# Performance work log

Measured on AMD Instinct MI355X. Metric: run time of the kernel, lower is better.

## Reference

```python
import jax, jax.numpy as jnp
import numpy as np
import math

N_HEADS = 16
N_BLOCK = 4
EPS = 1e-5


def _layernorm(h, g, b):
    mu = jnp.mean(h, axis=-1, keepdims=True)
    var = jnp.var(h, axis=-1, keepdims=True)
    return (h - mu) / jnp.sqrt(var + EPS) * g + b


def _sinusoidal_pe(S, D, dtype):
    pos = jnp.arange(S, dtype=jnp.float32)[:, None]                      # [S,1]
    div = jnp.exp(jnp.arange(0, D, 2, dtype=jnp.float32) * (-math.log(10000.0) / D))
    pe = jnp.zeros((S, D), dtype=jnp.float32)
    pe = pe.at[:, 0::2].set(jnp.sin(pos * div))
    pe = pe.at[:, 1::2].set(jnp.cos(pos * div))
    return pe.astype(dtype)


def setup_inputs() -> dict:
    key = jax.random.key(0)
    ks = jax.random.split(key, 10)
    V, D, Hf, B, S = 32000, 1024, 4096, 4, 1024
    s = 0.02
    return {
        'x': jax.random.randint(ks[0], (B, S), 0, V, dtype=jnp.int32),
        'emb_W': jax.random.normal(ks[1], (V, D), jnp.float32) * s,
        'q_W': jax.random.normal(ks[2], (D, D), jnp.float32) * s,
        'k_W': jax.random.normal(ks[3], (D, D), jnp.float32) * s,
        'v_W': jax.random.normal(ks[4], (D, D), jnp.float32) * s,
        'o_W': jax.random.normal(ks[5], (D, D), jnp.float32) * s,
        'ln0_g': jnp.ones((D,), jnp.float32),
        'ln0_b': jnp.zeros((D,), jnp.float32),
        'ln1_g': jnp.ones((D,), jnp.float32),
        'ln1_b': jnp.zeros((D,), jnp.float32),
        'ffn_W1': jax.random.normal(ks[6], (Hf, D), jnp.float32) * s,
        'ffn_b1': jnp.zeros((Hf,), jnp.float32),
        'ffn_W2': jax.random.normal(ks[7], (D, Hf), jnp.float32) * s,
        'ffn_b2': jnp.zeros((D,), jnp.float32),
        'out_W': jax.random.normal(ks[8], (V, D), jnp.float32) * s,
        'out_b': jnp.zeros((32000,), jnp.float32),
    }


def reference(x, emb_W, q_W, k_W, v_W, o_W, ln0_g, ln0_b, ln1_g, ln1_b,
              ffn_W1, ffn_b1, ffn_W2, ffn_b2, out_W, out_b):
    B, S = x.shape
    D = emb_W.shape[1]
    hd = D // N_HEADS
    # token embedding * sqrt(d_model) + sinusoidal PE (dropout is eval-mode identity)
    h = emb_W[x] * jnp.asarray(math.sqrt(D), emb_W.dtype)
    h = h + _sinusoidal_pe(S, D, h.dtype)[None]
    causal = jnp.tril(jnp.ones((S, S), dtype=bool))                      # [S,S]
    scale = 1.0 / math.sqrt(hd)

    for _ in range(N_BLOCK):  # weights shared across blocks, as in the source
        # attention sublayer; Resudial_Connections is x + LN(x)
        a_in = h + _layernorm(h, ln0_g, ln0_b)
        q = (a_in @ q_W.T).reshape(B, S, N_HEADS, hd).transpose(0, 2, 1, 3)
        k = (a_in @ k_W.T).reshape(B, S, N_HEADS, hd).transpose(0, 2, 1, 3)
        v = (a_in @ v_W.T).reshape(B, S, N_HEADS, hd).transpose(0, 2, 1, 3)
        scores = jnp.einsum('bhqd,bhkd->bhqk', q, k) * scale
        scores = jnp.where(causal, scores, -jnp.inf)
        attn = jax.nn.softmax(scores, axis=-1)
        o = jnp.einsum('bhqk,bhkd->bhqd', attn, v)
        o = o.transpose(0, 2, 1, 3).reshape(B, S, D) @ o_W.T
        h = h + o
        # FFN sublayer (intended Linear-ReLU-Linear)
        f_in = h + _layernorm(h, ln1_g, ln1_b)
        ff = jax.nn.relu(f_in @ ffn_W1.T + ffn_b1) @ ffn_W2.T + ffn_b2
        h = h + ff

    return h @ out_W.T + out_b                                           # [B,S,V]
```

## Files before the change

kernel.cpp:

```cpp
#include <hip/hip_runtime.h>
#include <hip/hip_bf16.h>
#include <math.h>

typedef __bf16 bf16_t;
typedef __bf16 bf16x8 __attribute__((ext_vector_type(8)));
typedef __bf16 bf16x4 __attribute__((ext_vector_type(4)));
typedef float  f32x4  __attribute__((ext_vector_type(4)));

#define MFMA_BF16(a, b, c) __builtin_amdgcn_mfma_f32_16x16x32_bf16((a), (b), (c), 0, 0, 0)

typedef const void __attribute__((address_space(1)))* gas_ptr;
typedef void       __attribute__((address_space(3)))* las_ptr;

__device__ __forceinline__ void gload_lds16(const void* g, void* l) {
  __builtin_amdgcn_global_load_lds((gas_ptr)g, (las_ptr)l, 16, 0, 0);
}

static constexpr int B_ = 4, S_ = 1024, D_ = 1024, HF_ = 4096, V_ = 32000;
static constexpr int NH_ = 16, HD_ = 64;
static constexpr int TOK_ = B_ * S_;

__global__ __launch_bounds__(256) void cvt_f32_bf16(const float* __restrict__ in,
                                                    bf16_t* __restrict__ out, int n4) {
  int i = blockIdx.x * 256 + threadIdx.x;
  if (i < n4) {
    float4 v = ((const float4*)in)[i];
    bf16x4 o;
    o[0] = (bf16_t)v.x; o[1] = (bf16_t)v.y; o[2] = (bf16_t)v.z; o[3] = (bf16_t)v.w;
    ((bf16x4*)out)[i] = o;
  }
}

__global__ __launch_bounds__(256) void pe_kernel(float* __restrict__ pe) {
  const int s = blockIdx.x;
  for (int i = threadIdx.x; i < D_ / 2; i += 256) {
    float div = expf((2.0f * (float)i) * (-9.210340371976184f / (float)D_));
    float a = (float)s * div;
    pe[(size_t)s * D_ + 2 * i]     = sinf(a);
    pe[(size_t)s * D_ + 2 * i + 1] = cosf(a);
  }
}

__global__ __launch_bounds__(256) void embed_kernel(const int* __restrict__ x,
                                                    const float* __restrict__ embW,
                                                    const float* __restrict__ pe,
                                                    float* __restrict__ h) {
  int i = blockIdx.x * 256 + threadIdx.x;
  int token = i >> 8;
  int c4 = i & 255;
  int idx = x[token];
  float4 e = ((const float4*)(embW + (size_t)idx * D_))[c4];
  float4 p = ((const float4*)(pe + (size_t)(token & (S_ - 1)) * D_))[c4];
  float4 o;
  o.x = e.x * 32.0f + p.x; o.y = e.y * 32.0f + p.y;
  o.z = e.z * 32.0f + p.z; o.w = e.w * 32.0f + p.w;
  ((float4*)(h + (size_t)token * D_))[c4] = o;
}

__global__ __launch_bounds__(256) void ln_res_kernel(const float* __restrict__ h,
                                                     const float* __restrict__ gamma,
                                                     const float* __restrict__ beta,
                                                     bf16_t* __restrict__ out) {
  const int row = blockIdx.x;
  const int tid = threadIdx.x;
  const float4 v = ((const float4*)(h + (size_t)row * D_))[tid];
  float s  = v.x + v.y + v.z + v.w;
  float s2 = v.x * v.x + v.y * v.y + v.z * v.z + v.w * v.w;
#pragma unroll
  for (int m = 1; m < 64; m <<= 1) {
    s  += __shfl_xor(s, m, 64);
    s2 += __shfl_xor(s2, m, 64);
  }
  __shared__ float red[2][4];
  const int wave = tid >> 6, lane = tid & 63;
  if (lane == 0) { red[0][wave] = s; red[1][wave] = s2; }
  __syncthreads();
  s  = red[0][0] + red[0][1] + red[0][2] + red[0][3];
  s2 = red[1][0] + red[1][1] + red[1][2] + red[1][3];
  const float mu   = s * (1.0f / D_);
  const float rstd = rsqrtf(s2 * (1.0f / D_) - mu * mu + 1e-5f);
  const float4 g4 = ((const float4*)gamma)[tid];
  const float4 b4 = ((const float4*)beta)[tid];
  bf16x4 o;
  o[0] = (bf16_t)(v.x + (v.x - mu) * rstd * g4.x + b4.x);
  o[1] = (bf16_t)(v.y + (v.y - mu) * rstd * g4.y + b4.y);
  o[2] = (bf16_t)(v.z + (v.z - mu) * rstd * g4.z + b4.z);
  o[3] = (bf16_t)(v.w + (v.w - mu) * rstd * g4.w + b4.w);
  ((bf16x4*)(out + (size_t)row * D_))[tid] = o;
}

template <int EPI>
__global__ __launch_bounds__(512, 4) void gemm_sq(
    const bf16_t* __restrict__ A, const bf16_t* __restrict__ W, int N, int K,
    float* __restrict__ fout, const float* __restrict__ bias, bf16_t* __restrict__ bout,
    bf16_t* __restrict__ qb, bf16_t* __restrict__ kb, bf16_t* __restrict__ vtb) {
  __shared__ char lds[2][32768];

  const int tid = threadIdx.x;
  const int wave = tid >> 6, lane = tid & 63;
  const int row16 = lane & 15, kgrp = lane >> 4;
  const int wm = wave >> 2, wn = wave & 3;

  const int nb = gridDim.x;
  const int logical = (blockIdx.x & 7) * (nb >> 3) + (blockIdx.x >> 3);
  const int m0 = (logical & 31) << 7;
  const int n0 = (logical >> 5) << 7;
  const size_t K2 = (size_t)K * 2;

  const int lr = lane >> 3;
  const int swz = ((lane & 7) * 16) ^ (lr << 4);
  const char* gA = (const char*)A + (size_t)(m0 + wave * 8 + lr) * K2 + swz;
  const char* gB = (const char*)W + (size_t)(n0 + wave * 8 + lr) * K2 + swz;
  char* const ldsc = &lds[0][0];
  const int dW = wave * 1024;

#define STG_A(v)                                                  \
  { char* d_ = ldsc + (((v) & 1) << 15) + dW;                     \
    const char* g_ = gA + (size_t)(v) * 128;                      \
    gload_lds16(g_, d_); gload_lds16(g_ + 64 * K2, d_ + 8192); }
#define STG_B(v)                                                  \
  { char* d_ = ldsc + (((v) & 1) << 15) + 16384 + dW;             \
    const char* g_ = gB + (size_t)(v) * 128;                      \
    gload_lds16(g_, d_); gload_lds16(g_ + 64 * K2, d_ + 8192); }

  const int colx0 = (kgrp * 16) ^ ((row16 & 7) << 4);
  const int colx1 = (64 + kgrp * 16) ^ ((row16 & 7) << 4);
  int aoff[4], boff[2];
#pragma unroll
  for (int mf = 0; mf < 4; mf++) aoff[mf] = (wm * 64 + mf * 16 + row16) * 128;
#pragma unroll
  for (int nf = 0; nf < 2; nf++) boff[nf] = 16384 + (nf * 64 + wn * 16 + row16) * 128;

#define GATE()                                        \
  __builtin_amdgcn_s_barrier();                       \
  asm volatile("s_waitcnt lgkmcnt(0)" ::: "memory");  \
  __builtin_amdgcn_sched_barrier(0);

  f32x4 acc[4][2] = {};
  bf16x8 af[4][2], bfr[2];
  const int NT = K >> 6;

  STG_A(0); STG_B(0); STG_A(1);
  asm volatile("s_waitcnt vmcnt(2)" ::: "memory");
  __builtin_amdgcn_s_barrier();

  for (int t = 0; t < NT; ++t) {
    const char* bufp = ldsc + ((t & 1) << 15);
#pragma unroll
    for (int mf = 0; mf < 4; mf++) {
      af[mf][0] = *(const bf16x8*)(bufp + aoff[mf] + colx0);
      af[mf][1] = *(const bf16x8*)(bufp + aoff[mf] + colx1);
    }
    bfr[0] = *(const bf16x8*)(bufp + boff[0] + colx0);
    bfr[1] = *(const bf16x8*)(bufp + boff[0] + colx1);
    if (t + 1 < NT) STG_B(t + 1);
    GATE();
    __builtin_amdgcn_s_setprio(1);
#pragma unroll
    for (int mf = 0; mf < 4; mf++) {
      acc[mf][0] = MFMA_BF16(af[mf][0], bfr[0], acc[mf][0]);
      acc[mf][0] = MFMA_BF16(af[mf][1], bfr[1], acc[mf][0]);
    }
    __builtin_amdgcn_s_setprio(0);
    __builtin_amdgcn_s_barrier();
    bfr[0] = *(const bf16x8*)(bufp + boff[1] + colx0);
    bfr[1] = *(const bf16x8*)(bufp + boff[1] + colx1);
    if (t + 2 < NT) STG_A(t + 2);
    GATE();
    __builtin_amdgcn_s_setprio(1);
#pragma unroll
    for (int mf = 0; mf < 4; mf++) {
      acc[mf][1] = MFMA_BF16(af[mf][0], bfr[0], acc[mf][1]);
      acc[mf][1] = MFMA_BF16(af[mf][1], bfr[1], acc[mf][1]);
    }
    __builtin_amdgcn_s_setprio(0);
    if (t + 2 < NT)      { asm volatile("s_waitcnt vmcnt(2)" ::: "memory"); }
    else if (t + 1 < NT) { asm volatile("s_waitcnt vmcnt(0)" ::: "memory"); }
    __builtin_amdgcn_s_barrier();
  }
#undef STG_A
#undef STG_B
#undef GATE

#pragma unroll
  for (int mf = 0; mf < 4; mf++) {
    const int rowb = m0 + wm * 64 + mf * 16 + kgrp * 4;
#pragma unroll
    for (int nf = 0; nf < 2; nf++) {
      const int col = n0 + nf * 64 + wn * 16 + row16;
#pragma unroll
      for (int r = 0; r < 4; r++) {
        const float v = acc[mf][nf][r];
        const int rr2 = rowb + r;
        if constexpr (EPI == 0) {
          const int bb = rr2 >> 10, s = rr2 & 1023;
          if (col < 1024) {
            const int hh = col >> 6, d = col & 63;
            qb[(((size_t)(bb * NH_ + hh)) * S_ + s) * HD_ + d] = (bf16_t)(v * 0.125f);
          } else if (col < 2048) {
            const int c = col - 1024, hh = c >> 6, d = c & 63;
            kb[(((size_t)(bb * NH_ + hh)) * S_ + s) * HD_ + d] = (bf16_t)v;
          } else {
            const int c = col - 2048, hh = c >> 6, d = c & 63;
            vtb[(((size_t)(bb * NH_ + hh)) * HD_ + d) * S_ + s] = (bf16_t)v;
          }
        } else if constexpr (EPI == 1) {
          fout[(size_t)rr2 * N + col] += v;
        } else if constexpr (EPI == 2) {
          bout[(size_t)rr2 * N + col] = (bf16_t)fmaxf(v + bias[col], 0.0f);
        } else {
          fout[(size_t)rr2 * N + col] += v + bias[col];
        }
      }
    }
  }
}

template <int EPI>
__global__ __launch_bounds__(512, 1) void gemm_pipe(
    const bf16_t* __restrict__ A, const bf16_t* __restrict__ W, int N, int K,
    float* __restrict__ fout, const float* __restrict__ bias) {
  __shared__ char lds[2][65536];

  const int tid = threadIdx.x;
  const int wave = tid >> 6, lane = tid & 63;
  const int row16 = lane & 15, kgrp = lane >> 4;
  const int wm = wave >> 2, wn = wave & 3;

  const int nb = gridDim.x;
  const int logical = (blockIdx.x & 7) * (nb >> 3) + (blockIdx.x >> 3);
  const int m0 = (logical & 15) << 8;
  const int n0 = (logical >> 4) << 8;
  const size_t K2 = (size_t)K * 2;

  const int lr = lane >> 3;
  const int swz = ((lane & 7) * 16) ^ (lr << 4);
  const int rA = wave * 8 + lr;
  const char* gAr = (const char*)A + (size_t)(m0 + rA) * K2 + swz;
  const int rB = (wave < 4 ? wave * 8 : 64 + (wave - 4) * 8) + lr;
  const char* gBr = (const char*)W + (size_t)(n0 + rB) * K2 + swz;
  char* const ldsc = &lds[0][0];
  const int dAw = wave * 1024;
  const int dBw = 32768 + (wave < 4 ? wave * 1024 : 8192 + (wave - 4) * 1024);

#define STG_AM03(v)                                                     \
  { char* d_ = ldsc + (((v) & 1) << 16) + dAw;                          \
    const char* g_ = gAr + (size_t)(v) * 128;                           \
    gload_lds16(g_, d_); gload_lds16(g_ + 128 * K2, d_ + 16384); }
#define STG_AM47(v)                                                     \
  { char* d_ = ldsc + (((v) & 1) << 16) + dAw + 8192;                   \
    const char* g_ = gAr + (size_t)(v) * 128 + 64 * K2;                 \
    gload_lds16(g_, d_); gload_lds16(g_ + 128 * K2, d_ + 16384); }
#define STG_BN01(v)                                                     \
  { char* d_ = ldsc + (((v) & 1) << 16) + dBw;                          \
    const char* g_ = gBr + (size_t)(v) * 128;                           \
    gload_lds16(g_, d_); gload_lds16(g_ + 128 * K2, d_ + 16384); }
#define STG_BN23(v)                                                     \
  { char* d_ = ldsc + (((v) & 1) << 16) + dBw + 4096;                   \
    const char* g_ = gBr + (size_t)(v) * 128 + 32 * K2;                 \
    gload_lds16(g_, d_); gload_lds16(g_ + 128 * K2, d_ + 16384); }

  const int colx0 = (kgrp * 16) ^ ((row16 & 7) << 4);
  const int colx1 = (64 + kgrp * 16) ^ ((row16 & 7) << 4);
  const int aA0 = (wm * 128 + row16) * 128 + colx0;
  const int aA1 = (wm * 128 + row16) * 128 + colx1;
  const int bA0 = 32768 + (wn * 64 + row16) * 128 + colx0;
  const int bA1 = 32768 + (wn * 64 + row16) * 128 + colx1;

#define LD_A(mh)                                                          \
  _Pragma("unroll") for (int m_ = 0; m_ < 4; m_++) {                      \
    af[m_][0] = *(const bf16x8*)(bufp + aA0 + (mh) * 8192 + m_ * 2048);   \
    af[m_][1] = *(const bf16x8*)(bufp + aA1 + (mh) * 8192 + m_ * 2048);   \
  }
#define LD_B(BF, nh)                                                      \
  _Pragma("unroll") for (int n_ = 0; n_ < 2; n_++) {                      \
    BF[n_][0] = *(const bf16x8*)(bufp + bA0 + (nh) * 4096 + n_ * 2048);   \
    BF[n_][1] = *(const bf16x8*)(bufp + bA1 + (nh) * 4096 + n_ * 2048);   \
  }
#define GATE()                                        \
  __builtin_amdgcn_s_barrier();                       \
  asm volatile("s_waitcnt lgkmcnt(0)" ::: "memory");  \
  __builtin_amdgcn_sched_barrier(0);
#define PH_MFMA(MB, NB, BF)                                                    \
  __builtin_amdgcn_s_setprio(1);                                               \
  _Pragma("unroll") for (int kh_ = 0; kh_ < 2; kh_++)                          \
    _Pragma("unroll") for (int m_ = 0; m_ < 4; m_++)                           \
      _Pragma("unroll") for (int n_ = 0; n_ < 2; n_++)                         \
          acc[(MB) + m_][(NB) + n_] =                                          \
              MFMA_BF16(af[m_][kh_], BF[n_][kh_], acc[(MB) + m_][(NB) + n_]);  \
  __builtin_amdgcn_s_setprio(0);

  f32x4 acc[8][4] = {};
  bf16x8 af[4][2], bfA[2][2], bfB[2][2];
  const int NT = K >> 6;

  STG_AM03(0); STG_BN01(0); STG_AM47(0); STG_BN23(0);
  if (NT > 1) { STG_AM03(1); STG_BN01(1); }
  if (NT > 1) { asm volatile("s_waitcnt vmcnt(8)" ::: "memory"); }
  else        { asm volatile("s_waitcnt vmcnt(4)" ::: "memory"); }
  __builtin_amdgcn_s_barrier();

  for (int t = 0; t < NT; ++t) {
    const char* bufp = ldsc + ((t & 1) << 16);
    LD_A(0);
    LD_B(bfA, 0);
    if (t + 1 < NT) STG_AM47(t + 1);
    GATE();
    PH_MFMA(0, 0, bfA);
    if (t + 1 < NT) { asm volatile("s_waitcnt vmcnt(6)" ::: "memory"); }
    else            { asm volatile("s_waitcnt vmcnt(0)" ::: "memory"); }
    __builtin_amdgcn_s_barrier();
    LD_B(bfB, 1);
    if (t + 1 < NT) STG_BN23(t + 1);
    GATE();
    PH_MFMA(0, 2, bfB);
    __builtin_amdgcn_s_barrier();
    LD_A(1);
    if (t + 2 < NT) STG_AM03(t + 2);
    GATE();
    PH_MFMA(4, 2, bfB);
    __builtin_amdgcn_s_barrier();
    if (t + 2 < NT) STG_BN01(t + 2);
    __builtin_amdgcn_s_barrier();
    __builtin_amdgcn_sched_barrier(0);
    PH_MFMA(4, 0, bfA);
    if (t + 2 < NT)      { asm volatile("s_waitcnt vmcnt(8)" ::: "memory"); }
    else if (t + 1 < NT) { asm volatile("s_waitcnt vmcnt(4)" ::: "memory"); }
    __builtin_amdgcn_s_barrier();
  }
#undef STG_AM03
#undef STG_AM47
#undef STG_BN01
#undef STG_BN23
#undef LD_A
#undef LD_B
#undef GATE
#undef PH_MFMA

#pragma unroll
  for (int m = 0; m < 8; m++) {
    const int rowb = m0 + wm * 128 + m * 16 + kgrp * 4;
#pragma unroll
    for (int n = 0; n < 4; n++) {
      const int col = n0 + wn * 64 + n * 16 + row16;
#pragma unroll
      for (int r = 0; r < 4; r++) {
        fout[(size_t)(rowb + r) * N + col] = acc[m][n][r] + bias[col];
      }
    }
  }
}

__global__ __launch_bounds__(256, 3) void attn_flash(const bf16_t* __restrict__ qg,
                                                     const bf16_t* __restrict__ kg,
                                                     const bf16_t* __restrict__ vtg,
                                                     bf16_t* __restrict__ aout) {
  const int nb = gridDim.x;
  const int logical = ((blockIdx.x & 7) * (nb >> 3)) + (blockIdx.x >> 3);
  const int qtile = logical & 15;
  const int bh    = logical >> 4;
  const int tid = threadIdx.x;
  const int wave = tid >> 6, lane = tid & 63;
  const int row16 = lane & 15, kgrp = lane >> 4;
  const int q0 = qtile * 64 + wave * 16;

  const bf16_t* qb = qg + (size_t)bh * S_ * HD_;
  const bf16_t* kb = kg + (size_t)bh * S_ * HD_;
  const bf16_t* vb = vtg + (size_t)bh * HD_ * S_;

  const bf16x8 qf0 = *(const bf16x8*)&qb[(size_t)(q0 + row16) * HD_ + kgrp * 8];
  const bf16x8 qf1 = *(const bf16x8*)&qb[(size_t)(q0 + row16) * HD_ + 32 + kgrp * 8];

  f32x4 accO[4] = {};
  float mrun[4] = {-1e30f, -1e30f, -1e30f, -1e30f};
  float lrun[4] = {0.f, 0.f, 0.f, 0.f};

  __shared__ char sP[4][2048];
  char* const sw = &sP[wave][0];

  const int NTt = qtile + 1;

  bf16x8 kf[4][2];
#pragma unroll
  for (int q = 0; q < 4; q++) {
    kf[q][0] = *(const bf16x8*)&kb[(size_t)(q * 16 + row16) * HD_ + kgrp * 8];
    kf[q][1] = *(const bf16x8*)&kb[(size_t)(q * 16 + row16) * HD_ + 32 + kgrp * 8];
  }

  for (int t = 0; t < NTt; ++t) {
    const int k0 = t * 64;
    f32x4 sc[4];
#pragma unroll
    for (int q = 0; q < 4; q++) {
      f32x4 z = {};
      z = MFMA_BF16(qf0, kf[q][0], z);
      sc[q] = MFMA_BF16(qf1, kf[q][1], z);
    }
    bf16x8 vf[4][2];
#pragma unroll
    for (int d = 0; d < 4; d++) {
      vf[d][0] = *(const bf16x8*)&vb[(size_t)(d * 16 + row16) * S_ + k0 + kgrp * 8];
      vf[d][1] = *(const bf16x8*)&vb[(size_t)(d * 16 + row16) * S_ + k0 + 32 + kgrp * 8];
    }
    const bool diag = (k0 + 64 > q0);
    float p[4][4];
#pragma unroll
    for (int r = 0; r < 4; r++) {
      const int qglob = q0 + kgrp * 4 + r;
      float s0 = sc[0][r], s1 = sc[1][r], s2 = sc[2][r], s3 = sc[3][r];
      if (diag) {
        s0 = (k0 + row16 <= qglob) ? s0 : -1e30f;
        s1 = (k0 + 16 + row16 <= qglob) ? s1 : -1e30f;
        s2 = (k0 + 32 + row16 <= qglob) ? s2 : -1e30f;
        s3 = (k0 + 48 + row16 <= qglob) ? s3 : -1e30f;
      }
      float tmax = fmaxf(fmaxf(s0, s1), fmaxf(s2, s3));
#pragma unroll
      for (int msk = 1; msk < 16; msk <<= 1) tmax = fmaxf(tmax, __shfl_xor(tmax, msk, 64));
      const float mnew  = fmaxf(mrun[r], tmax);
      const float alpha = __expf(mrun[r] - mnew);
      const float e0 = __expf(s0 - mnew);
      const float e1 = __expf(s1 - mnew);
      const float e2 = __expf(s2 - mnew);
      const float e3 = __expf(s3 - mnew);
      float ls = (e0 + e1) + (e2 + e3);
#pragma unroll
      for (int msk = 1; msk < 16; msk <<= 1) ls += __shfl_xor(ls, msk, 64);
      lrun[r] = lrun[r] * alpha + ls;
      mrun[r] = mnew;
#pragma unroll
      for (int d = 0; d < 4; d++) accO[d][r] *= alpha;
      p[r][0] = e0; p[r][1] = e1; p[r][2] = e2; p[r][3] = e3;
    }
    if (t + 1 < NTt) {
      const int k0n = k0 + 64;
#pragma unroll
      for (int q = 0; q < 4; q++) {
        kf[q][0] = *(const bf16x8*)&kb[(size_t)(k0n + q * 16 + row16) * HD_ + kgrp * 8];
        kf[q][1] = *(const bf16x8*)&kb[(size_t)(k0n + q * 16 + row16) * HD_ + 32 + kgrp * 8];
      }
    }
#pragma unroll
    for (int r = 0; r < 4; r++) {
      const int prow = kgrp * 4 + r;
      const int px = (prow & 7) << 4;
#pragma unroll
      for (int q = 0; q < 4; q++) {
        *(bf16_t*)(sw + prow * 128 + (((q * 16 + row16) * 2) ^ px)) = (bf16_t)p[r][q];
      }
    }
    const int rx = (row16 & 7) << 4;
    const bf16x8 pf0 = *(const bf16x8*)(sw + row16 * 128 + ((kgrp * 16) ^ rx));
    const bf16x8 pf1 = *(const bf16x8*)(sw + row16 * 128 + ((64 + kgrp * 16) ^ rx));
#pragma unroll
    for (int d = 0; d < 4; d++) {
      accO[d] = MFMA_BF16(pf0, vf[d][0], accO[d]);
      accO[d] = MFMA_BF16(pf1, vf[d][1], accO[d]);
    }
  }

  const int b = bh >> 4, hh = bh & 15;
#pragma unroll
  for (int d = 0; d < 4; d++)
#pragma unroll
    for (int r = 0; r < 4; r++) {
      const int tok = b * S_ + q0 + kgrp * 4 + r;
      aout[(size_t)tok * D_ + hh * HD_ + d * 16 + row16] = (bf16_t)(accO[d][r] / lrun[r]);
    }
}

extern "C" void kernel_launch(void* const* d_in, const int* in_sizes, int n_in,
                              void* d_out, int out_size, void* d_ws, size_t ws_size,
                              hipStream_t stream) {
  const int*   x      = (const int*)d_in[0];
  const float* emb_W  = (const float*)d_in[1];
  const float* q_W    = (const float*)d_in[2];
  const float* k_W    = (const float*)d_in[3];
  const float* v_W    = (const float*)d_in[4];
  const float* o_W    = (const float*)d_in[5];
  const float* ln0_g  = (const float*)d_in[6];
  const float* ln0_b  = (const float*)d_in[7];
  const float* ln1_g  = (const float*)d_in[8];
  const float* ln1_b  = (const float*)d_in[9];
  const float* ffn_W1 = (const float*)d_in[10];
  const float* ffn_b1 = (const float*)d_in[11];
  const float* ffn_W2 = (const float*)d_in[12];
  const float* ffn_b2 = (const float*)d_in[13];
  const float* out_W  = (const float*)d_in[14];
  const float* out_b  = (const float*)d_in[15];
  float* out = (float*)d_out;

  char* p = (char*)d_ws;
  auto take = [&](size_t n) { char* r = p; p += (n + 255) & ~(size_t)255; return r; };
  float*  pe    = (float*)take((size_t)S_ * D_ * 4);
  float*  h     = (float*)take((size_t)TOK_ * D_ * 4);
  bf16_t* ain   = (bf16_t*)take((size_t)TOK_ * D_ * 2);
  bf16_t* attno = (bf16_t*)take((size_t)TOK_ * D_ * 2);
  bf16_t* qb    = (bf16_t*)take((size_t)B_ * NH_ * S_ * HD_ * 2);
  bf16_t* kb    = (bf16_t*)take((size_t)B_ * NH_ * S_ * HD_ * 2);
  bf16_t* vtb   = (bf16_t*)take((size_t)B_ * NH_ * S_ * HD_ * 2);
  bf16_t* ff    = (bf16_t*)take((size_t)TOK_ * HF_ * 2);
  bf16_t* qkvW  = (bf16_t*)take((size_t)3 * D_ * D_ * 2);
  bf16_t* oWb   = (bf16_t*)take((size_t)D_ * D_ * 2);
  bf16_t* W1b   = (bf16_t*)take((size_t)HF_ * D_ * 2);
  bf16_t* W2b   = (bf16_t*)take((size_t)D_ * HF_ * 2);
  bf16_t* outWb = (bf16_t*)take((size_t)V_ * D_ * 2);

  cvt_f32_bf16<<<1024, 256, 0, stream>>>(q_W, qkvW, D_ * D_ / 4);
  cvt_f32_bf16<<<1024, 256, 0, stream>>>(k_W, qkvW + (size_t)D_ * D_, D_ * D_ / 4);
  cvt_f32_bf16<<<1024, 256, 0, stream>>>(v_W, qkvW + (size_t)2 * D_ * D_, D_ * D_ / 4);
  cvt_f32_bf16<<<1024, 256, 0, stream>>>(o_W, oWb, D_ * D_ / 4);
  cvt_f32_bf16<<<4096, 256, 0, stream>>>(ffn_W1, W1b, HF_ * D_ / 4);
  cvt_f32_bf16<<<4096, 256, 0, stream>>>(ffn_W2, W2b, D_ * HF_ / 4);
  cvt_f32_bf16<<<32000, 256, 0, stream>>>(out_W, outWb, V_ * D_ / 4);

  pe_kernel<<<S_, 256, 0, stream>>>(pe);
  embed_kernel<<<TOK_ * D_ / 4 / 256, 256, 0, stream>>>(x, emb_W, pe, h);

  for (int blk = 0; blk < 4; blk++) {
    ln_res_kernel<<<TOK_, 256, 0, stream>>>(h, ln0_g, ln0_b, ain);
    gemm_sq<0><<<32 * (3 * D_ / 128), 512, 0, stream>>>(
        ain, qkvW, 3 * D_, D_, nullptr, nullptr, nullptr, qb, kb, vtb);
    attn_flash<<<16 * B_ * NH_, 256, 0, stream>>>(qb, kb, vtb, attno);
    gemm_sq<1><<<32 * (D_ / 128), 512, 0, stream>>>(
        attno, oWb, D_, D_, h, nullptr, nullptr, nullptr, nullptr, nullptr);
    ln_res_kernel<<<TOK_, 256, 0, stream>>>(h, ln1_g, ln1_b, ain);
    gemm_sq<2><<<32 * (HF_ / 128), 512, 0, stream>>>(
        ain, W1b, HF_, D_, nullptr, ffn_b1, ff, nullptr, nullptr, nullptr);
    gemm_sq<3><<<32 * (D_ / 128), 512, 0, stream>>>(
        ff, W2b, D_, HF_, h, ffn_b2, nullptr, nullptr, nullptr, nullptr);
  }

  cvt_f32_bf16<<<4096, 256, 0, stream>>>(h, ain, TOK_ * D_ / 4);
  gemm_pipe<4><<<16 * (V_ / 256), 512, 0, stream>>>(
      ain, outWb, V_, D_, out, out_b);
}
```

Measured before the change: 1.537 ms.

## Replace pipelined vocab GEMM with gemm_sq and compute softmax row sums via MFMA

Removes the specialized 256x256 gemm_pipe kernel and runs the final vocab projection through the generic gemm_sq template, adding an EPI=4 store-with-bias epilogue. In flash attention, the per-row sum of exponentials is now accumulated by MFMA against a vector of ones instead of cross-lane shuffle reductions. The final normalization uses a reciprocal multiply. The row sums now come from the bf16-rounded probabilities, which matches the values used for P·V. The larger vocab GEMM may lose the tuned pipelining and the bigger tile reuse it had before.

Result: slower. 1.652 ms (+7.5%).

```diff
diff --git a/kernel.cpp b/kernel.cpp
--- a/kernel.cpp
+++ b/kernel.cpp
@@ -208,144 +208,11 @@
           fout[(size_t)rr2 * N + col] += v;
         } else if constexpr (EPI == 2) {
           bout[(size_t)rr2 * N + col] = (bf16_t)fmaxf(v + bias[col], 0.0f);
+        } else if constexpr (EPI == 3) {
+          fout[(size_t)rr2 * N + col] += v + bias[col];
         } else {
-          fout[(size_t)rr2 * N + col] += v + bias[col];
+          fout[(size_t)rr2 * N + col] = v + bias[col];
         }
-      }
-    }
-  }
-}
-
-template <int EPI>
-__global__ __launch_bounds__(512, 1) void gemm_pipe(
-    const bf16_t* __restrict__ A, const bf16_t* __restrict__ W, int N, int K,
-    float* __restrict__ fout, const float* __restrict__ bias) {
-  __shared__ char lds[2][65536];
-
-  const int tid = threadIdx.x;
-  const int wave = tid >> 6, lane = tid & 63;
-  const int row16 = lane & 15, kgrp = lane >> 4;
-  const int wm = wave >> 2, wn = wave & 3;
-
-  const int nb = gridDim.x;
-  const int logical = (blockIdx.x & 7) * (nb >> 3) + (blockIdx.x >> 3);
-  const int m0 = (logical & 15) << 8;
-  const int n0 = (logical >> 4) << 8;
-  const size_t K2 = (size_t)K * 2;
-
-  const int lr = lane >> 3;
-  const int swz = ((lane & 7) * 16) ^ (lr << 4);
-  const int rA = wave * 8 + lr;
-  const char* gAr = (const char*)A + (size_t)(m0 + rA) * K2 + swz;
-  const int rB = (wave < 4 ? wave * 8 : 64 + (wave - 4) * 8) + lr;
-  const char* gBr = (const char*)W + (size_t)(n0 + rB) * K2 + swz;
-  char* const ldsc = &lds[0][0];
-  const int dAw = wave * 1024;
-  const int dBw = 32768 + (wave < 4 ? wave * 1024 : 8192 + (wave - 4) * 1024);
-
-#define STG_AM03(v)                                                     \
-  { char* d_ = ldsc + (((v) & 1) << 16) + dAw;                          \
-    const char* g_ = gAr + (size_t)(v) * 128;                           \
-    gload_lds16(g_, d_); gload_lds16(g_ + 128 * K2, d_ + 16384); }
-#define STG_AM47(v)                                                     \
-  { char* d_ = ldsc + (((v) & 1) << 16) + dAw + 8192;                   \
-    const char* g_ = gAr + (size_t)(v) * 128 + 64 * K2;                 \
-    gload_lds16(g_, d_); gload_lds16(g_ + 128 * K2, d_ + 16384); }
-#define STG_BN01(v)                                                     \
-  { char* d_ = ldsc + (((v) & 1) << 16) + dBw;                          \
-    const char* g_ = gBr + (size_t)(v) * 128;                           \
-    gload_lds16(g_, d_); gload_lds16(g_ + 128 * K2, d_ + 16384); }
-#define STG_BN23(v)                                                     \
-  { char* d_ = ldsc + (((v) & 1) << 16) + dBw + 4096;                   \
-    const char* g_ = gBr + (size_t)(v) * 128 + 32 * K2;                 \
-    gload_lds16(g_, d_); gload_lds16(g_ + 128 * K2, d_ + 16384); }
-
-  const int colx0 = (kgrp * 16) ^ ((row16 & 7) << 4);
-  const int colx1 = (64 + kgrp * 16) ^ ((row16 & 7) << 4);
-  const int aA0 = (wm * 128 + row16) * 128 + colx0;
-  const int aA1 = (wm * 128 + row16) * 128 + colx1;
-  const int bA0 = 32768 + (wn * 64 + row16) * 128 + colx0;
-  const int bA1 = 32768 + (wn * 64 + row16) * 128 + colx1;
-
-#define LD_A(mh)                                                          \
-  _Pragma("unroll") for (int m_ = 0; m_ < 4; m_++) {                      \
-    af[m_][0] = *(const bf16x8*)(bufp + aA0 + (mh) * 8192 + m_ * 2048);   \
-    af[m_][1] = *(const bf16x8*)(bufp + aA1 + (mh) * 8192 + m_ * 2048);   \
-  }
-#define LD_B(BF, nh)                                                      \
-  _Pragma("unroll") for (int n_ = 0; n_ < 2; n_++) {                      \
-    BF[n_][0] = *(const bf16x8*)(bufp + bA0 + (nh) * 4096 + n_ * 2048);   \
-    BF[n_][1] = *(const bf16x8*)(bufp + bA1 + (nh) * 4096 + n_ * 2048);   \
-  }
-#define GATE()                                        \
-  __builtin_amdgcn_s_barrier();                       \
-  asm volatile("s_waitcnt lgkmcnt(0)" ::: "memory");  \
-  __builtin_amdgcn_sched_barrier(0);
-#define PH_MFMA(MB, NB, BF)                                                    \
-  __builtin_amdgcn_s_setprio(1);                                               \
-  _Pragma("unroll") for (int kh_ = 0; kh_ < 2; kh_++)                          \
-    _Pragma("unroll") for (int m_ = 0; m_ < 4; m_++)                           \
-      _Pragma("unroll") for (int n_ = 0; n_ < 2; n_++)                         \
-          acc[(MB) + m_][(NB) + n_] =                                          \
-              MFMA_BF16(af[m_][kh_], BF[n_][kh_], acc[(MB) + m_][(NB) + n_]);  \
-  __builtin_amdgcn_s_setprio(0);
-
-  f32x4 acc[8][4] = {};
-  bf16x8 af[4][2], bfA[2][2], bfB[2][2];
-  const int NT = K >> 6;
-
-  STG_AM03(0); STG_BN01(0); STG_AM47(0); STG_BN23(0);
-  if (NT > 1) { STG_AM03(1); STG_BN01(1); }
-  if (NT > 1) { asm volatile("s_waitcnt vmcnt(8)" ::: "memory"); }
-  else        { asm volatile("s_waitcnt vmcnt(4)" ::: "memory"); }
-  __builtin_amdgcn_s_barrier();
-
-  for (int t = 0; t < NT; ++t) {
-    const char* bufp = ldsc + ((t & 1) << 16);
-    LD_A(0);
-    LD_B(bfA, 0);
-    if (t + 1 < NT) STG_AM47(t + 1);
-    GATE();
-    PH_MFMA(0, 0, bfA);
-    if (t + 1 < NT) { asm volatile("s_waitcnt vmcnt(6)" ::: "memory"); }
-    else            { asm volatile("s_waitcnt vmcnt(0)" ::: "memory"); }
-    __builtin_amdgcn_s_barrier();
-    LD_B(bfB, 1);
-    if (t + 1 < NT) STG_BN23(t + 1);
-    GATE();
-    PH_MFMA(0, 2, bfB);
-    __builtin_amdgcn_s_barrier();
-    LD_A(1);
-    if (t + 2 < NT) STG_AM03(t + 2);
-    GATE();
-    PH_MFMA(4, 2, bfB);
-    __builtin_amdgcn_s_barrier();
-    if (t + 2 < NT) STG_BN01(t + 2);
-    __builtin_amdgcn_s_barrier();
-    __builtin_amdgcn_sched_barrier(0);
-    PH_MFMA(4, 0, bfA);
-    if (t + 2 < NT)      { asm volatile("s_waitcnt vmcnt(8)" ::: "memory"); }
-    else if (t + 1 < NT) { asm volatile("s_waitcnt vmcnt(4)" ::: "memory"); }
-    __builtin_amdgcn_s_barrier();
-  }
-#undef STG_AM03
-#undef STG_AM47
-#undef STG_BN01
-#undef STG_BN23
-#undef LD_A
-#undef LD_B
-#undef GATE
-#undef PH_MFMA
-
-#pragma unroll
-  for (int m = 0; m < 8; m++) {
-    const int rowb = m0 + wm * 128 + m * 16 + kgrp * 4;
-#pragma unroll
-    for (int n = 0; n < 4; n++) {
-      const int col = n0 + wn * 64 + n * 16 + row16;
-#pragma unroll
-      for (int r = 0; r < 4; r++) {
-        fout[(size_t)(rowb + r) * N + col] = acc[m][n][r] + bias[col];
       }
     }
   }
@@ -372,8 +239,12 @@
   const bf16x8 qf1 = *(const bf16x8*)&qb[(size_t)(q0 + row16) * HD_ + 32 + kgrp * 8];
 
   f32x4 accO[4] = {};
+  f32x4 accL = {};
   float mrun[4] = {-1e30f, -1e30f, -1e30f, -1e30f};
-  float lrun[4] = {0.f, 0.f, 0.f, 0.f};
+
+  bf16x8 ones;
+#pragma unroll
+  for (int i = 0; i < 8; i++) ones[i] = (bf16_t)1.0f;
 
   __shared__ char sP[4][2048];
   char* const sw = &sP[wave][0];
@@ -419,18 +290,14 @@
       for (int msk = 1; msk < 16; msk <<= 1) tmax = fmaxf(tmax, __shfl_xor(tmax, msk, 64));
       const float mnew  = fmaxf(mrun[r], tmax);
       const float alpha = __expf(mrun[r] - mnew);
-      const float e0 = __expf(s0 - mnew);
-      const float e1 = __expf(s1 - mnew);
-      const float e2 = __expf(s2 - mnew);
-      const float e3 = __expf(s3 - mnew);
-      float ls = (e0 + e1) + (e2 + e3);
-#pragma unroll
-      for (int msk = 1; msk < 16; msk <<= 1) ls += __shfl_xor(ls, msk, 64);
-      lrun[r] = lrun[r] * alpha + ls;
       mrun[r] = mnew;
+      p[r][0] = __expf(s0 - mnew);
+      p[r][1] = __expf(s1 - mnew);
+      p[r][2] = __expf(s2 - mnew);
+      p[r][3] = __expf(s3 - mnew);
+      accL[r] *= alpha;
 #pragma unroll
       for (int d = 0; d < 4; d++) accO[d][r] *= alpha;
-      p[r][0] = e0; p[r][1] = e1; p[r][2] = e2; p[r][3] = e3;
     }
     if (t + 1 < NTt) {
       const int k0n = k0 + 64;
@@ -452,6 +319,8 @@
     const int rx = (row16 & 7) << 4;
     const bf16x8 pf0 = *(const bf16x8*)(sw + row16 * 128 + ((kgrp * 16) ^ rx));
     const bf16x8 pf1 = *(const bf16x8*)(sw + row16 * 128 + ((64 + kgrp * 16) ^ rx));
+    accL = MFMA_BF16(pf0, ones, accL);
+    accL = MFMA_BF16(pf1, ones, accL);
 #pragma unroll
     for (int d = 0; d < 4; d++) {
       accO[d] = MFMA_BF16(pf0, vf[d][0], accO[d]);
@@ -459,13 +328,16 @@
     }
   }
 
+  float rinv[4];
+#pragma unroll
+  for (int r = 0; r < 4; r++) rinv[r] = 1.0f / accL[r];
   const int b = bh >> 4, hh = bh & 15;
 #pragma unroll
   for (int d = 0; d < 4; d++)
 #pragma unroll
     for (int r = 0; r < 4; r++) {
       const int tok = b * S_ + q0 + kgrp * 4 + r;
-      aout[(size_t)tok * D_ + hh * HD_ + d * 16 + row16] = (bf16_t)(accO[d][r] / lrun[r]);
+      aout[(size_t)tok * D_ + hh * HD_ + d * 16 + row16] = (bf16_t)(accO[d][r] * rinv[r]);
     }
 }
 
@@ -532,6 +404,6 @@
   }
 
   cvt_f32_bf16<<<4096, 256, 0, stream>>>(h, ain, TOK_ * D_ / 4);
-  gemm_pipe<4><<<16 * (V_ / 256), 512, 0, stream>>>(
-      ain, outWb, V_, D_, out, out_b);
-}
+  gemm_sq<4><<<32 * (V_ / 128), 512, 0, stream>>>(
+      ain, outWb, V_, D_, out, out_b, nullptr, nullptr, nullptr, nullptr);
+}
```
